# Kernel tuning notes

Measured on AMD Instinct MI355X. Metric: run time of the kernel, lower is better.

## Reference

```python
import jax, jax.numpy as jnp
import numpy as np
from jax import lax

K = 4
OUT_PLANES = 128
TEMPERATURE = 30.0


def setup_inputs() -> dict:
    key = jax.random.key(0)
    ks = jax.random.split(key, 5)
    in_planes, k = 128, 3
    he_std = float(np.sqrt(2.0)) * (in_planes * k * k) ** (-0.5)
    return {
        "x": jax.random.normal(ks[0], (16, in_planes, 64, 64), jnp.float32),
        "weight": jax.random.normal(ks[1], (K * OUT_PLANES, in_planes, k, k), jnp.float32) * he_std,
        "bias": jax.random.normal(ks[2], (K * OUT_PLANES,), jnp.float32) * 0.01,
        "se_w1": jax.random.normal(ks[3], (33, in_planes), jnp.float32) * (2.0 / 33) ** 0.5,
        "se_w2": jax.random.normal(ks[4], (K, 33), jnp.float32) * (2.0 / K) ** 0.5,
        "se_b2": jnp.zeros((K,), jnp.float32),
    }


def reference(x, weight, bias, se_w1, se_w2, se_b2):
    B = x.shape[0]
    # SE attention: global avg pool -> fc1 -> relu -> fc2 -> softmax(./T)
    pooled = x.mean(axis=(2, 3))                      # [B, Cin]
    h = jax.nn.relu(pooled @ se_w1.T)                 # [B, hidden]
    logits = h @ se_w2.T + se_b2                      # [B, K]
    attn = jax.nn.softmax(logits / TEMPERATURE, axis=1)
    # conv with K*out channels (groups=1, stride=1, pad=1, dil=1)
    y = lax.conv_general_dilated(
        x, weight, window_strides=(1, 1), padding=[(1, 1), (1, 1)],
        dimension_numbers=("NCHW", "OIHW", "NCHW"))
    y = y + bias[None, :, None, None]                 # [B, K*out, Ho, Wo]
    Ho, Wo = y.shape[2], y.shape[3]
    y = y.reshape(B, K, OUT_PLANES, Ho, Wo)
    # attention-weighted combine over K branches (bmm in torch)
    return jnp.einsum("bk,bkohw->bohw", attn, y)
```

## Files before the change

### kernel.cpp

```cpp
#include <hip/hip_runtime.h>
#include <cstdint>
#include <cstddef>

typedef unsigned short u16;
typedef __attribute__((ext_vector_type(8))) short short8;
typedef __attribute__((ext_vector_type(4))) float f32x4;

__device__ __forceinline__ u16 f2bf(float f){
  union { float f; unsigned u; } c; c.f = f;
  unsigned u = c.u;
  u += 0x7fffu + ((u >> 16) & 1u);
  return (u16)(u >> 16);
}
__device__ __forceinline__ unsigned pk2(float a, float b){
  union { float f; unsigned u; } ca, cb; ca.f = a; cb.f = b;
  return ((ca.u + 0x8000u) >> 16) | ((cb.u + 0x8000u) & 0xFFFF0000u);
}

#define XB_STRIDE 557568
#define XR_STRIDE 8448


#define GLD_LDS(gsrc, ldst) \
  __builtin_amdgcn_global_load_lds((const __attribute__((address_space(1))) void*)(gsrc), \
                                   (__attribute__((address_space(3))) void*)(ldst), 16, 0, 0)

#define BAR { asm volatile("s_waitcnt lgkmcnt(0)" ::: "memory"); \
              __builtin_amdgcn_s_barrier(); }
#define WAIT_VM(N) asm volatile("s_waitcnt vmcnt(" #N ")" ::: "memory")

__global__ __launch_bounds__(256) void xpose_pool(
    const float* __restrict__ x, u16* __restrict__ xT2, float* __restrict__ part)
{
  const int bid = blockIdx.x;
  const int b = bid & 15, chunk = bid >> 4;
  const int pos0 = chunk << 6;
  const int tid = threadIdx.x;
  __shared__ u16 tile[8192];
  __shared__ float psum[128 * 17];
  const float* xb = x + ((size_t)b << 19) + pos0;
  const int rq = tid & 15;
  const int p4 = rq << 2;
  const int gci = tid >> 4;

  if (chunk == 0){
    u16* xh = xT2 + (size_t)b * XB_STRIDE;
    for (int i = tid; i < 4160; i += 256){
      const int p = i >> 4, oct = i & 15;
      int row, col;
      if (p < 66)      { row = 0;        col = p; }
      else if (p < 132){ row = 65;       col = p - 66; }
      else if (p < 196){ row = p - 131;  col = 0; }
      else             { row = p - 195;  col = 65; }
      *(uint4*)(xh + row * XR_STRIDE + (col << 7) + (oct << 3)) =
          make_uint4(0u, 0u, 0u, 0u);
    }
  }

  {
    const int ci8 = gci << 3;
    float4 L[8];
    #pragma unroll
    for (int j = 0; j < 8; ++j)
      L[j] = *(const float4*)(xb + ((size_t)(ci8 + j) << 12) + p4);
    #pragma unroll
    for (int j = 0; j < 8; ++j)
      psum[(ci8 + j) * 17 + rq] = L[j].x + L[j].y + L[j].z + L[j].w;
    const int gs = gci ^ (rq & 7);
    const float* e = (const float*)L;
    #pragma unroll
    for (int p = 0; p < 4; ++p){
      const int row = p4 + p;
      uint4 V;
      V.x = pk2(e[0 * 4 + p], e[1 * 4 + p]);
      V.y = pk2(e[2 * 4 + p], e[3 * 4 + p]);
      V.z = pk2(e[4 * 4 + p], e[5 * 4 + p]);
      V.w = pk2(e[6 * 4 + p], e[7 * 4 + p]);
      *(uint4*)(tile + (row << 7) + (gs << 3)) = V;
    }
  }
  __syncthreads();

  if (tid < 128){
    float s = 0.f;
    #pragma unroll
    for (int j = 0; j < 16; ++j) s += psum[tid * 17 + j];
    part[(((b << 6) | chunk) << 7) + tid] = s;
  }

  u16* xo = xT2 + (size_t)b * XB_STRIDE;
  const int g = tid & 15, rb = (tid >> 4) << 2;
  #pragma unroll
  for (int r = 0; r < 4; ++r){
    const int row = rb + r;
    const int gs = g ^ ((row >> 2) & 7);
    uint4 v = *(const uint4*)(tile + (row << 7) + (gs << 3));
    const int pos = pos0 + row;
    const int h = pos >> 6, w = pos & 63;
    *(uint4*)(xo + (h + 1) * XR_STRIDE + ((w + 1) << 7) + (g << 3)) = v;
  }
}

__global__ __launch_bounds__(256) void combine(
    const float* __restrict__ W, const float* __restrict__ bias,
    const float* __restrict__ part, const float* __restrict__ w1,
    const float* __restrict__ w2, const float* __restrict__ b2,
    u16* __restrict__ wcomb, float* __restrict__ bcomb)
{
  __shared__ float wlds[9216];
  __shared__ float sp[128];
  __shared__ float sh[33];
  __shared__ float sat[4];
  const int bid = blockIdx.x;
  const int b = bid & 15, cp = bid >> 4;
  const int tid = threadIdx.x;

  #pragma unroll
  for (int it = 0; it < 9; ++it){
    const int G = it * 256 + tid;
    const int k = G / 576, rem = G - k * 576;
    const int co_l = rem / 288, j4 = rem - co_l * 288;
    const float* src = W + (size_t)(k * 128 + (cp << 1) + co_l) * 1152 + (j4 << 2);
    GLD_LDS(src, (char*)wlds + (G << 4));
  }

  if (tid < 128){
    const float* pb = part + (b << 13);
    float s = 0.f;
    #pragma unroll 8
    for (int c = 0; c < 64; ++c) s += pb[(c << 7) + tid];
    sp[tid] = s * (1.f / 4096.f);
  }
  __syncthreads();
  if (tid < 33){
    float h = 0.f;
    for (int ci = 0; ci < 128; ++ci) h += sp[ci] * w1[tid * 128 + ci];
    sh[tid] = fmaxf(h, 0.f);
  }
  __syncthreads();
  if (tid == 0){
    float l[4];
    #pragma unroll
    for (int t = 0; t < 4; ++t){
      float v = b2[t];
      for (int j = 0; j < 33; ++j) v += sh[j] * w2[t * 33 + j];
      l[t] = v * (1.f / 30.f);
    }
    float m = fmaxf(fmaxf(l[0], l[1]), fmaxf(l[2], l[3]));
    float e0 = __expf(l[0] - m), e1 = __expf(l[1] - m);
    float e2 = __expf(l[2] - m), e3 = __expf(l[3] - m);
    float inv = 1.f / (e0 + e1 + e2 + e3);
    sat[0] = e0 * inv; sat[1] = e1 * inv; sat[2] = e2 * inv; sat[3] = e3 * inv;
  }
  asm volatile("s_waitcnt vmcnt(0)" ::: "memory");
  __syncthreads();
  const float a0 = sat[0], a1 = sat[1], a2 = sat[2], a3 = sat[3];

  if (tid < 2){
    const int co = (cp << 1) + tid;
    bcomb[(b << 7) + co] = a0 * bias[co] + a1 * bias[128 + co]
                         + a2 * bias[256 + co] + a3 * bias[384 + co];
  }

  u16* wob = wcomb + (size_t)b * 147456;
  for (int gi = tid; gi < 288; gi += 256){
    const int co_l = gi / 144;
    const int r = gi - co_l * 144;
    const int tap = r >> 4;
    const int gg = r & 15;
    const int q = gg >> 2, g = gg & 3;
    const int co = (cp << 1) + co_l;
    union { u16 h[8]; uint4 v; } pk;
    #pragma unroll
    for (int e = 0; e < 8; ++e){
      const int ci = (q << 5) + (g << 3) + e;
      const int j = ci * 9 + tap;
      float s = a0 * wlds[co_l * 1152 + j]        + a1 * wlds[2304 + co_l * 1152 + j]
              + a2 * wlds[4608 + co_l * 1152 + j] + a3 * wlds[6912 + co_l * 1152 + j];
      pk.h[e] = f2bf(s);
    }
    *(uint4*)(wob + (((tap << 2) + q) << 12) + (co << 5) + (g << 3)) = pk.v;
  }
}

__global__ __launch_bounds__(256, 2) void conv_mfma(
    const u16* __restrict__ xT2, const u16* __restrict__ wcomb,
    const float* __restrict__ bcomb, float* __restrict__ out)
{
  extern __shared__ char smem[];
  u16* s_x = (u16*)smem;
  u16* s_w = (u16*)(smem + 33792);

  const int tid = threadIdx.x;
  const int lane = tid & 63, wid = tid >> 6;
  const int wr = wid & 1, wcv = wid >> 1;
  const int l15 = lane & 15, hi = lane >> 4;

  const int bid = blockIdx.x;
  const int b = bid & 15;
  const int h0 = (bid >> 4) << 1;

  const u16* Abase = wcomb + (size_t)b * 147456;
  const u16* Xbase = xT2 + (size_t)b * XB_STRIDE;

#define STAGE_X(Q) { \
    u16* _sx = s_x + ((Q) & 1) * 8448; \
    _Pragma("unroll") \
    for (int _it = 0; _it < 5; ++_it){ \
      const int _G = _it * 256 + tid; \
      if (_it < 4 || _G < 1056){ \
        const int _oct = _G & 3, _t = _G >> 2; \
        const int _col = _t % 66, _row = _t / 66; \
        const u16* _src = Xbase + (h0 + _row) * XR_STRIDE + (_col << 7) \
                        + ((Q) << 5) + (_oct << 3); \
        GLD_LDS(_src, _sx + (_G << 3)); \
      } \
    } }

#define STAGE_W(Q, TAP, BUF) { \
    const u16* _As = Abase + ((((TAP) << 2) + (Q)) << 12); \
    u16* _sw = s_w + (BUF) * 4096; \
    GLD_LDS(_As + (tid << 3), _sw + (tid << 3)); \
    GLD_LDS(_As + ((tid + 256) << 3), _sw + ((tid + 256) << 3)); }

#define COMPUTE(Q, TAP, BUF) { \
    const int _dh = (TAP) / 3, _dw = (TAP) - 3 * (_dh); \
    const u16* _sw = s_w + (BUF) * 4096; \
    const u16* _sx = s_x + ((Q) & 1) * 8448; \
    short8 _af[4], _bf[4]; \
    _Pragma("unroll") \
    for (int _a = 0; _a < 4; ++_a){ \
      const int _co = (wcv << 6) + (_a << 4) + l15; \
      _af[_a] = *(const short8*)(_sw + (_co << 5) + (hi << 3)); \
    } \
    _Pragma("unroll") \
    for (int _p = 0; _p < 4; ++_p){ \
      const int _col = l15 + _dw + (_p << 4); \
      _bf[_p] = *(const short8*)(_sx + (((wr + _dh) * 66 + _col) << 5) + (hi << 3)); \
    } \
    _Pragma("unroll") \
    for (int _a = 0; _a < 4; ++_a) \
      _Pragma("unroll") \
      for (int _p = 0; _p < 4; ++_p) \
        acc[_a][_p] = __builtin_amdgcn_mfma_f32_16x16x32_bf16(_af[_a], _bf[_p], acc[_a][_p], 0, 0, 0); }

  f32x4 acc[4][4] = {};

  STAGE_X(0);
  STAGE_W(0, 0, 0);
  STAGE_W(0, 1, 1);

  for (int q = 0; q < 4; ++q){
    #pragma unroll
    for (int tap = 0; tap < 9; ++tap){
      if (q == 3 && tap == 8)                  { WAIT_VM(0); }
      else if (q < 3 && (tap == 6 || tap == 7)){ WAIT_VM(11); }
      else                                     { WAIT_VM(2); }
      BAR;
      if (tap <= 6){
        STAGE_W(q, tap + 2, (tap + 2) % 3);
      } else if (tap == 7){
        if (q < 3){ STAGE_W(q + 1, 0, 0); }
      } else {
        if (q < 3){ STAGE_W(q + 1, 1, 1); }
      }
      if (tap == 5 && q < 3){ STAGE_X(q + 1); }
      __builtin_amdgcn_s_setprio(1);
      COMPUTE(q, tap, tap % 3);
      __builtin_amdgcn_s_setprio(0);
    }
  }

#undef COMPUTE
#undef STAGE_W
#undef STAGE_X

  const int hrow = h0 + wr;
  float* ob = out + ((size_t)b << 19) + (hrow << 6) + l15;
  #pragma unroll
  for (int a = 0; a < 4; ++a){
    const int co0 = (wcv << 6) + (a << 4) + (hi << 2);
    #pragma unroll
    for (int r = 0; r < 4; ++r){
      const float bc = bcomb[(b << 7) + co0 + r];
      float* op = ob + (size_t)(co0 + r) * 4096;
      #pragma unroll
      for (int p = 0; p < 4; ++p)
        __builtin_nontemporal_store(acc[a][p][r] + bc, op + (p << 4));
    }
  }
}

extern "C" void kernel_launch(void* const* d_in, const int* in_sizes, int n_in,
                              void* d_out, int out_size, void* d_ws, size_t ws_size,
                              hipStream_t stream)
{
  const float* x    = (const float*)d_in[0];
  const float* W    = (const float*)d_in[1];
  const float* bias = (const float*)d_in[2];
  const float* w1   = (const float*)d_in[3];
  const float* w2   = (const float*)d_in[4];
  const float* b2   = (const float*)d_in[5];
  float* out = (float*)d_out;

  char* ws = (char*)d_ws;
  float* part  = (float*)(ws);
  float* bcomb = (float*)(ws + 524288);
  u16*   xT2   = (u16*)  (ws + 532480);
  u16*   wcomb = (u16*)  (ws + 18374656);

  xpose_pool<<<1024, 256, 0, stream>>>(x, xT2, part);
  combine<<<1024, 256, 0, stream>>>(W, bias, part, w1, w2, b2, wcomb, bcomb);

  (void)hipFuncSetAttribute(reinterpret_cast<const void*>(conv_mfma),
                            hipFuncAttributeMaxDynamicSharedMemorySize, 58368);
  conv_mfma<<<512, 256, 58368, stream>>>(xT2, wcomb, bcomb, out);
}
```

Measured before the change: 49.04 us.

## Re-layout activations and combined weights into channel-slot planes for conflict-free LDS reads

Changes the transposed activation buffer from [row][col][128 channels] to [row][16 channel-slots][col][8 channels]. It also changes the combined weight buffer to [tap,q][group][co][8], and updates the producer kernels, the staging address math and the MFMA fragment reads to match. Consecutive lanes now read adjacent 16-byte chunks from LDS instead of 64-byte-strided ones, which is meant to remove LDS bank conflicts in the inner MFMA loop. The vmcnt wait before the tap-6/7 barriers is tightened from 11 to 6, which makes more outstanding loads complete earlier and may reduce overlap.

```diff
diff --git a/kernel.cpp b/kernel.cpp
--- a/kernel.cpp
+++ b/kernel.cpp
@@ -18,7 +18,8 @@
 }
 
 #define XB_STRIDE 557568
-#define XR_STRIDE 8448
+#define XROW 8448
+#define XSLOT 528
 
 
 #define GLD_LDS(gsrc, ldst) \
@@ -33,8 +34,8 @@
     const float* __restrict__ x, u16* __restrict__ xT2, float* __restrict__ part)
 {
   const int bid = blockIdx.x;
-  const int b = bid & 15, chunk = bid >> 4;
-  const int pos0 = chunk << 6;
+  const int b = bid & 15, h = bid >> 4;
+  const int pos0 = h << 6;
   const int tid = threadIdx.x;
   __shared__ u16 tile[8192];
   __shared__ float psum[128 * 17];
@@ -43,16 +44,16 @@
   const int p4 = rq << 2;
   const int gci = tid >> 4;
 
-  if (chunk == 0){
+  if (h == 0){
     u16* xh = xT2 + (size_t)b * XB_STRIDE;
     for (int i = tid; i < 4160; i += 256){
-      const int p = i >> 4, oct = i & 15;
+      const int p = i >> 4, slot = i & 15;
       int row, col;
       if (p < 66)      { row = 0;        col = p; }
       else if (p < 132){ row = 65;       col = p - 66; }
       else if (p < 196){ row = p - 131;  col = 0; }
       else             { row = p - 195;  col = 65; }
-      *(uint4*)(xh + row * XR_STRIDE + (col << 7) + (oct << 3)) =
+      *(uint4*)(xh + row * XROW + slot * XSLOT + (col << 3)) =
           make_uint4(0u, 0u, 0u, 0u);
     }
   }
@@ -70,13 +71,13 @@
     const float* e = (const float*)L;
     #pragma unroll
     for (int p = 0; p < 4; ++p){
-      const int row = p4 + p;
+      const int w = p4 + p;
       uint4 V;
       V.x = pk2(e[0 * 4 + p], e[1 * 4 + p]);
       V.y = pk2(e[2 * 4 + p], e[3 * 4 + p]);
       V.z = pk2(e[4 * 4 + p], e[5 * 4 + p]);
       V.w = pk2(e[6 * 4 + p], e[7 * 4 + p]);
-      *(uint4*)(tile + (row << 7) + (gs << 3)) = V;
+      *(uint4*)(tile + (w << 7) + (gs << 3)) = V;
     }
   }
   __syncthreads();
@@ -85,19 +86,19 @@
     float s = 0.f;
     #pragma unroll
     for (int j = 0; j < 16; ++j) s += psum[tid * 17 + j];
-    part[(((b << 6) | chunk) << 7) + tid] = s;
-  }
-
-  u16* xo = xT2 + (size_t)b * XB_STRIDE;
-  const int g = tid & 15, rb = (tid >> 4) << 2;
-  #pragma unroll
-  for (int r = 0; r < 4; ++r){
-    const int row = rb + r;
-    const int gs = g ^ ((row >> 2) & 7);
-    uint4 v = *(const uint4*)(tile + (row << 7) + (gs << 3));
-    const int pos = pos0 + row;
-    const int h = pos >> 6, w = pos & 63;
-    *(uint4*)(xo + (h + 1) * XR_STRIDE + ((w + 1) << 7) + (g << 3)) = v;
+    part[(((b << 6) | h) << 7) + tid] = s;
+  }
+
+  {
+    u16* xo = xT2 + (size_t)b * XB_STRIDE + (size_t)(h + 1) * XROW;
+    const int g = tid & 15, colq = tid >> 4;
+    const int gs = g ^ (colq & 7);
+    #pragma unroll
+    for (int c = 0; c < 4; ++c){
+      const int w = (colq << 2) + c;
+      uint4 v = *(const uint4*)(tile + (w << 7) + (gs << 3));
+      *(uint4*)(xo + g * XSLOT + ((w + 1) << 3)) = v;
+    }
   }
 }
 
@@ -179,7 +180,7 @@
               + a2 * wlds[4608 + co_l * 1152 + j] + a3 * wlds[6912 + co_l * 1152 + j];
       pk.h[e] = f2bf(s);
     }
-    *(uint4*)(wob + (((tap << 2) + q) << 12) + (co << 5) + (g << 3)) = pk.v;
+    *(uint4*)(wob + (((tap << 2) + q) << 12) + (g << 10) + (co << 3)) = pk.v;
   }
 }
 
@@ -209,10 +210,10 @@
     for (int _it = 0; _it < 5; ++_it){ \
       const int _G = _it * 256 + tid; \
       if (_it < 4 || _G < 1056){ \
-        const int _oct = _G & 3, _t = _G >> 2; \
-        const int _col = _t % 66, _row = _t / 66; \
-        const u16* _src = Xbase + (h0 + _row) * XR_STRIDE + (_col << 7) \
-                        + ((Q) << 5) + (_oct << 3); \
+        const int _t = _G / 66, _col = _G - _t * 66; \
+        const int _row = _t >> 2, _slot = _t & 3; \
+        const u16* _src = Xbase + (h0 + _row) * XROW \
+                        + ((((Q) << 2) + _slot) * XSLOT) + (_col << 3); \
         GLD_LDS(_src, _sx + (_G << 3)); \
       } \
     } }
@@ -231,12 +232,12 @@
     _Pragma("unroll") \
     for (int _a = 0; _a < 4; ++_a){ \
       const int _co = (wcv << 6) + (_a << 4) + l15; \
-      _af[_a] = *(const short8*)(_sw + (_co << 5) + (hi << 3)); \
+      _af[_a] = *(const short8*)(_sw + (hi << 10) + (_co << 3)); \
     } \
     _Pragma("unroll") \
     for (int _p = 0; _p < 4; ++_p){ \
       const int _col = l15 + _dw + (_p << 4); \
-      _bf[_p] = *(const short8*)(_sx + (((wr + _dh) * 66 + _col) << 5) + (hi << 3)); \
+      _bf[_p] = *(const short8*)(_sx + (((((wr + _dh) << 2) + hi) * 66 + _col) << 3)); \
     } \
     _Pragma("unroll") \
     for (int _a = 0; _a < 4; ++_a) \
@@ -254,7 +255,7 @@
     #pragma unroll
     for (int tap = 0; tap < 9; ++tap){
       if (q == 3 && tap == 8)                  { WAIT_VM(0); }
-      else if (q < 3 && (tap == 6 || tap == 7)){ WAIT_VM(11); }
+      else if (q < 3 && (tap == 6 || tap == 7)){ WAIT_VM(6); }
       else                                     { WAIT_VM(2); }
       BAR;
       if (tap <= 6){
```

After: 52.68 us. 1.07x slower.
